# Performance work log

Measured on AMD Instinct MI355X. Metric: run time of the kernel, lower is better.

Reference implementation:

```python
import jax, jax.numpy as jnp
import numpy as np

B, T, H = 32, 4096, 1024

def setup_inputs() -> dict:
    key = jax.random.key(0)
    k1, k2 = jax.random.split(key)
    decoder_state = jax.random.normal(k1, (B, H), dtype=jnp.float32)
    encoder_hiddens = jax.random.normal(k2, (B, T, H), dtype=jnp.float32)
    return {"decoder_state": decoder_state, "encoder_hiddens": encoder_hiddens}

def reference(decoder_state, encoder_hiddens):
    # Faithful to the original: torch.sum(s_t * h_t) reduces over batch AND
    # hidden, so score[:, t] is one scalar broadcast to every batch row.
    # scores: [T]
    scores = jnp.einsum('bh,bth->t', decoder_state, encoder_hiddens)
    batch_size = encoder_hiddens.shape[0]
    attention_score = jnp.broadcast_to(scores[None, :], (batch_size, scores.shape[0]))
    attention_distribution = jax.nn.softmax(attention_score, axis=1)  # [B, T]
    # context_vector[b] = sum_t dist[b, t] * encoder_hiddens[b, t]
    context_vector = jnp.einsum('bt,bth->bh', attention_distribution, encoder_hiddens)
    return context_vector
```

## Files before the change

kernel.cpp:

```cpp
#include <hip/hip_runtime.h>
#include <math.h>

#define B_  32
#define T_  4096
#define H_  1024
#define H4_ 256
#define G_  256
#define TPG_ (T_ / G_)
#define BH4_ (B_ * H4_)

__global__ __launch_bounds__(1024) void flash_kernel(
    const float4* __restrict__ s4, const float4* __restrict__ eh4,
    float4* __restrict__ Og4, float* __restrict__ mg, float* __restrict__ lg)
{
    const int g    = blockIdx.x;
    const int tid  = threadIdx.x;
    const int lane = tid & 63;
    const int w    = tid >> 6;
    const int b    = tid >> 5;
    const int hb   = tid & 31;

    __shared__ float redw[16];
    __shared__ float sc_sh;

    float4 sreg[8];
#pragma unroll
    for (int j = 0; j < 8; ++j)
        sreg[j] = s4[b * H4_ + hb + 32 * j];

    const float4* ep = eh4 + ((size_t)b * T_ + (size_t)g * TPG_) * H4_ + hb;

    float4 acc[8];
#pragma unroll
    for (int j = 0; j < 8; ++j) acc[j] = make_float4(0.f, 0.f, 0.f, 0.f);
    float m = -INFINITY, l = 0.f;

    for (int i = 0; i < TPG_; ++i) {
        float4 e[8];
#pragma unroll
        for (int j = 0; j < 8; ++j) e[j] = ep[32 * j];
        ep += H4_;

        float p = 0.f;
#pragma unroll
        for (int j = 0; j < 8; ++j)
            p += e[j].x * sreg[j].x + e[j].y * sreg[j].y
               + e[j].z * sreg[j].z + e[j].w * sreg[j].w;

        for (int off = 32; off > 0; off >>= 1)
            p += __shfl_down(p, off, 64);
        if (lane == 0) redw[w] = p;
        __syncthreads();
        if (w == 0) {
            float q = (lane < 16) ? redw[lane] : 0.f;
            q += __shfl_down(q, 8, 64);
            q += __shfl_down(q, 4, 64);
            q += __shfl_down(q, 2, 64);
            q += __shfl_down(q, 1, 64);
            if (lane == 0) sc_sh = q;
        }
        __syncthreads();
        const float score = sc_sh;

        const float mn    = fmaxf(m, score);
        const float alpha = __expf(m - mn);
        const float wgt   = __expf(score - mn);
        l = l * alpha + wgt;
#pragma unroll
        for (int j = 0; j < 8; ++j) {
            acc[j].x = acc[j].x * alpha + wgt * e[j].x;
            acc[j].y = acc[j].y * alpha + wgt * e[j].y;
            acc[j].z = acc[j].z * alpha + wgt * e[j].z;
            acc[j].w = acc[j].w * alpha + wgt * e[j].w;
        }
        m = mn;
    }

    float4* op = Og4 + (size_t)g * BH4_ + b * H4_ + hb;
#pragma unroll
    for (int j = 0; j < 8; ++j) op[32 * j] = acc[j];
    if (tid == 0) { mg[g] = m; lg[g] = l; }
}

__global__ __launch_bounds__(64) void combine_kernel(
    const float4* __restrict__ Og4, const float* __restrict__ mg,
    const float* __restrict__ lg, float4* __restrict__ out4)
{
    const int tid = threadIdx.x;
    __shared__ float wsh[G_];

    float mv[4];
    float M = -INFINITY;
#pragma unroll
    for (int j = 0; j < 4; ++j) {
        mv[j] = mg[tid + 64 * j];
        M = fmaxf(M, mv[j]);
    }
    for (int off = 32; off > 0; off >>= 1)
        M = fmaxf(M, __shfl_down(M, off, 64));
    M = __shfl(M, 0, 64);

    float Ls = 0.f;
#pragma unroll
    for (int j = 0; j < 4; ++j)
        Ls += lg[tid + 64 * j] * __expf(mv[j] - M);
    for (int off = 32; off > 0; off >>= 1)
        Ls += __shfl_down(Ls, off, 64);
    Ls = __shfl(Ls, 0, 64);
    const float invL = 1.f / Ls;

#pragma unroll
    for (int j = 0; j < 4; ++j)
        wsh[tid + 64 * j] = __expf(mv[j] - M) * invL;
    __syncthreads();

    const int o4 = blockIdx.x * 64 + tid;
    float4 acc = make_float4(0.f, 0.f, 0.f, 0.f);
    for (int gg = 0; gg < G_; gg += 4) {
        float4 a0 = Og4[(size_t)(gg + 0) * BH4_ + o4];
        float4 a1 = Og4[(size_t)(gg + 1) * BH4_ + o4];
        float4 a2 = Og4[(size_t)(gg + 2) * BH4_ + o4];
        float4 a3 = Og4[(size_t)(gg + 3) * BH4_ + o4];
        float w0 = wsh[gg], w1 = wsh[gg + 1], w2 = wsh[gg + 2], w3 = wsh[gg + 3];
        acc.x += w0 * a0.x + w1 * a1.x + w2 * a2.x + w3 * a3.x;
        acc.y += w0 * a0.y + w1 * a1.y + w2 * a2.y + w3 * a3.y;
        acc.z += w0 * a0.z + w1 * a1.z + w2 * a2.z + w3 * a3.z;
        acc.w += w0 * a0.w + w1 * a1.w + w2 * a2.w + w3 * a3.w;
    }
    out4[o4] = acc;
}

extern "C" void kernel_launch(void* const* d_in, const int* in_sizes, int n_in,
                              void* d_out, int out_size, void* d_ws, size_t ws_size,
                              hipStream_t stream) {
    const float* s  = (const float*)d_in[0];
    const float* eh = (const float*)d_in[1];

    float4* Og4 = (float4*)d_ws;
    float*  mg  = (float*)(Og4 + (size_t)G_ * BH4_);
    float*  lg  = mg + G_;

    flash_kernel<<<G_, 1024, 0, stream>>>(
        (const float4*)s, (const float4*)eh, Og4, mg, lg);
    combine_kernel<<<BH4_ / 64, 64, 0, stream>>>(
        Og4, mg, lg, (float4*)d_out);
}
```

Before: 697.4 us.

## Pipeline score reduction with next-row prefetch, single barrier, and split combine

The flash kernel now makes each wavefront own two batch rows. It prefetches the next time step's encoder row into registers while the current row, staged in LDS, updates the accumulators. The two-barrier block reduction becomes one barrier over a double-buffered per-wave partial array that every thread reads and sums itself. The combine step is split into two kernels: one reduces chunks of partial outputs across many blocks, a second sums the chunks and normalises. This replaces the former 128-block combine that read all 256 partials serially. The changes add 128KB of LDS per block and an extra launch and workspace buffer.

```diff
diff --git a/kernel.cpp b/kernel.cpp
--- a/kernel.cpp
+++ b/kernel.cpp
@@ -1,13 +1,15 @@
 #include <hip/hip_runtime.h>
 #include <math.h>
 
-#define B_  32
-#define T_  4096
-#define H_  1024
-#define H4_ 256
-#define G_  256
+#define B_   32
+#define T_   4096
+#define H_   1024
+#define H4_  256
+#define G_   256
 #define TPG_ (T_ / G_)
 #define BH4_ (B_ * H4_)
+#define NCHUNK_ 8
+#define GPC_ (G_ / NCHUNK_)
 
 __global__ __launch_bounds__(1024) void flash_kernel(
     const float4* __restrict__ s4, const float4* __restrict__ eh4,
@@ -17,117 +19,185 @@
     const int tid  = threadIdx.x;
     const int lane = tid & 63;
     const int w    = tid >> 6;
-    const int b    = tid >> 5;
-    const int hb   = tid & 31;
-
-    __shared__ float redw[16];
-    __shared__ float sc_sh;
-
-    float4 sreg[8];
-#pragma unroll
-    for (int j = 0; j < 8; ++j)
-        sreg[j] = s4[b * H4_ + hb + 32 * j];
-
-    const float4* ep = eh4 + ((size_t)b * T_ + (size_t)g * TPG_) * H4_ + hb;
-
-    float4 acc[8];
-#pragma unroll
-    for (int j = 0; j < 8; ++j) acc[j] = make_float4(0.f, 0.f, 0.f, 0.f);
+    const int b0   = w * 2;
+    const int b1   = b0 + 1;
+
+    __shared__ float4 elds[B_ * H4_];
+    __shared__ __align__(16) float redw[2][16];
+
+    float4 sA[4], sB[4];
+#pragma unroll
+    for (int j = 0; j < 4; ++j) {
+        sA[j] = s4[b0 * H4_ + lane + 64 * j];
+        sB[j] = s4[b1 * H4_ + lane + 64 * j];
+    }
+
+    const float4* epA = eh4 + ((size_t)b0 * T_ + (size_t)g * TPG_) * H4_ + lane;
+    const float4* epB = eh4 + ((size_t)b1 * T_ + (size_t)g * TPG_) * H4_ + lane;
+    float4* slotA = &elds[b0 * H4_ + lane];
+    float4* slotB = &elds[b1 * H4_ + lane];
+
+    float pdot;
+    {
+        float4 eA[4], eB[4];
+#pragma unroll
+        for (int j = 0; j < 4; ++j) { eA[j] = epA[64 * j]; eB[j] = epB[64 * j]; }
+        epA += H4_; epB += H4_;
+        float p = 0.f;
+#pragma unroll
+        for (int j = 0; j < 4; ++j) {
+            p += eA[j].x * sA[j].x + eA[j].y * sA[j].y
+               + eA[j].z * sA[j].z + eA[j].w * sA[j].w;
+            p += eB[j].x * sB[j].x + eB[j].y * sB[j].y
+               + eB[j].z * sB[j].z + eB[j].w * sB[j].w;
+        }
+        pdot = p;
+#pragma unroll
+        for (int j = 0; j < 4; ++j) { slotA[64 * j] = eA[j]; slotB[64 * j] = eB[j]; }
+    }
+
+    float4 accA[4], accB[4];
+#pragma unroll
+    for (int j = 0; j < 4; ++j) {
+        accA[j] = make_float4(0.f, 0.f, 0.f, 0.f);
+        accB[j] = make_float4(0.f, 0.f, 0.f, 0.f);
+    }
     float m = -INFINITY, l = 0.f;
 
-    for (int i = 0; i < TPG_; ++i) {
-        float4 e[8];
-#pragma unroll
-        for (int j = 0; j < 8; ++j) e[j] = ep[32 * j];
-        ep += H4_;
-
-        float p = 0.f;
-#pragma unroll
-        for (int j = 0; j < 8; ++j)
-            p += e[j].x * sreg[j].x + e[j].y * sreg[j].y
-               + e[j].z * sreg[j].z + e[j].w * sreg[j].w;
-
+    for (int t = 0; t < TPG_; ++t) {
+        float4 eA[4], eB[4];
+        if (t < TPG_ - 1) {
+#pragma unroll
+            for (int j = 0; j < 4; ++j) { eA[j] = epA[64 * j]; eB[j] = epB[64 * j]; }
+            epA += H4_; epB += H4_;
+        }
+
+        float q = pdot;
         for (int off = 32; off > 0; off >>= 1)
-            p += __shfl_down(p, off, 64);
-        if (lane == 0) redw[w] = p;
-        __syncthreads();
-        if (w == 0) {
-            float q = (lane < 16) ? redw[lane] : 0.f;
-            q += __shfl_down(q, 8, 64);
-            q += __shfl_down(q, 4, 64);
-            q += __shfl_down(q, 2, 64);
-            q += __shfl_down(q, 1, 64);
-            if (lane == 0) sc_sh = q;
-        }
-        __syncthreads();
-        const float score = sc_sh;
+            q += __shfl_down(q, off, 64);
+        if (lane == 0) redw[t & 1][w] = q;
+        asm volatile("s_waitcnt lgkmcnt(0)" ::: "memory");
+        __builtin_amdgcn_sched_barrier(0);
+        __builtin_amdgcn_s_barrier();
+        __builtin_amdgcn_sched_barrier(0);
+        asm volatile("" ::: "memory");
+
+        const float4* rp = (const float4*)&redw[t & 1][0];
+        float4 r0 = rp[0], r1 = rp[1], r2 = rp[2], r3 = rp[3];
+        const float score = ((r0.x + r0.y) + (r0.z + r0.w))
+                          + ((r1.x + r1.y) + (r1.z + r1.w))
+                          + ((r2.x + r2.y) + (r2.z + r2.w))
+                          + ((r3.x + r3.y) + (r3.z + r3.w));
 
         const float mn    = fmaxf(m, score);
         const float alpha = __expf(m - mn);
         const float wgt   = __expf(score - mn);
         l = l * alpha + wgt;
-#pragma unroll
-        for (int j = 0; j < 8; ++j) {
-            acc[j].x = acc[j].x * alpha + wgt * e[j].x;
-            acc[j].y = acc[j].y * alpha + wgt * e[j].y;
-            acc[j].z = acc[j].z * alpha + wgt * e[j].z;
-            acc[j].w = acc[j].w * alpha + wgt * e[j].w;
-        }
         m = mn;
-    }
-
-    float4* op = Og4 + (size_t)g * BH4_ + b * H4_ + hb;
-#pragma unroll
-    for (int j = 0; j < 8; ++j) op[32 * j] = acc[j];
+
+#pragma unroll
+        for (int j = 0; j < 4; ++j) {
+            float4 vA = slotA[64 * j];
+            accA[j].x = accA[j].x * alpha + wgt * vA.x;
+            accA[j].y = accA[j].y * alpha + wgt * vA.y;
+            accA[j].z = accA[j].z * alpha + wgt * vA.z;
+            accA[j].w = accA[j].w * alpha + wgt * vA.w;
+            float4 vB = slotB[64 * j];
+            accB[j].x = accB[j].x * alpha + wgt * vB.x;
+            accB[j].y = accB[j].y * alpha + wgt * vB.y;
+            accB[j].z = accB[j].z * alpha + wgt * vB.z;
+            accB[j].w = accB[j].w * alpha + wgt * vB.w;
+        }
+
+        if (t < TPG_ - 1) {
+            float p1 = 0.f;
+#pragma unroll
+            for (int j = 0; j < 4; ++j) {
+                p1 += eA[j].x * sA[j].x + eA[j].y * sA[j].y
+                    + eA[j].z * sA[j].z + eA[j].w * sA[j].w;
+                p1 += eB[j].x * sB[j].x + eB[j].y * sB[j].y
+                    + eB[j].z * sB[j].z + eB[j].w * sB[j].w;
+            }
+            pdot = p1;
+#pragma unroll
+            for (int j = 0; j < 4; ++j) { slotA[64 * j] = eA[j]; slotB[64 * j] = eB[j]; }
+        }
+    }
+
+    float4* opA = Og4 + (size_t)g * BH4_ + b0 * H4_ + lane;
+    float4* opB = Og4 + (size_t)g * BH4_ + b1 * H4_ + lane;
+#pragma unroll
+    for (int j = 0; j < 4; ++j) { opA[64 * j] = accA[j]; opB[64 * j] = accB[j]; }
     if (tid == 0) { mg[g] = m; lg[g] = l; }
 }
 
-__global__ __launch_bounds__(64) void combine_kernel(
+__global__ __launch_bounds__(256) void combine_a(
     const float4* __restrict__ Og4, const float* __restrict__ mg,
+    float4* __restrict__ p2)
+{
+    const int tid = threadIdx.x;
+    const int oc  = blockIdx.x & 31;
+    const int gc  = blockIdx.x >> 5;
+    __shared__ float wsh[GPC_];
+    __shared__ float red[4];
+
+    float mv = mg[tid];
+    float M = mv;
+    for (int off = 32; off > 0; off >>= 1)
+        M = fmaxf(M, __shfl_down(M, off, 64));
+    if ((tid & 63) == 0) red[tid >> 6] = M;
+    __syncthreads();
+    M = fmaxf(fmaxf(red[0], red[1]), fmaxf(red[2], red[3]));
+    __syncthreads();
+
+    if (tid < GPC_) wsh[tid] = __expf(mg[gc * GPC_ + tid] - M);
+    __syncthreads();
+
+    const int o4 = oc * 256 + tid;
+    const float4* src = Og4 + (size_t)(gc * GPC_) * BH4_ + o4;
+    float4 acc = make_float4(0.f, 0.f, 0.f, 0.f);
+#pragma unroll 8
+    for (int gg = 0; gg < GPC_; ++gg) {
+        float4 a = src[(size_t)gg * BH4_];
+        float wv = wsh[gg];
+        acc.x += wv * a.x; acc.y += wv * a.y;
+        acc.z += wv * a.z; acc.w += wv * a.w;
+    }
+    p2[(size_t)gc * BH4_ + o4] = acc;
+}
+
+__global__ __launch_bounds__(256) void combine_b(
+    const float4* __restrict__ p2, const float* __restrict__ mg,
     const float* __restrict__ lg, float4* __restrict__ out4)
 {
     const int tid = threadIdx.x;
-    __shared__ float wsh[G_];
-
-    float mv[4];
-    float M = -INFINITY;
-#pragma unroll
-    for (int j = 0; j < 4; ++j) {
-        mv[j] = mg[tid + 64 * j];
-        M = fmaxf(M, mv[j]);
-    }
+    __shared__ float red[4];
+
+    float mv = mg[tid];
+    float M = mv;
     for (int off = 32; off > 0; off >>= 1)
         M = fmaxf(M, __shfl_down(M, off, 64));
-    M = __shfl(M, 0, 64);
-
-    float Ls = 0.f;
-#pragma unroll
-    for (int j = 0; j < 4; ++j)
-        Ls += lg[tid + 64 * j] * __expf(mv[j] - M);
+    if ((tid & 63) == 0) red[tid >> 6] = M;
+    __syncthreads();
+    M = fmaxf(fmaxf(red[0], red[1]), fmaxf(red[2], red[3]));
+    __syncthreads();
+
+    float Ls = lg[tid] * __expf(mv - M);
     for (int off = 32; off > 0; off >>= 1)
         Ls += __shfl_down(Ls, off, 64);
-    Ls = __shfl(Ls, 0, 64);
-    const float invL = 1.f / Ls;
-
-#pragma unroll
-    for (int j = 0; j < 4; ++j)
-        wsh[tid + 64 * j] = __expf(mv[j] - M) * invL;
-    __syncthreads();
-
-    const int o4 = blockIdx.x * 64 + tid;
+    if ((tid & 63) == 0) red[tid >> 6] = Ls;
+    __syncthreads();
+    const float invL = 1.f / ((red[0] + red[1]) + (red[2] + red[3]));
+
+    const int o4 = blockIdx.x * 256 + tid;
     float4 acc = make_float4(0.f, 0.f, 0.f, 0.f);
-    for (int gg = 0; gg < G_; gg += 4) {
-        float4 a0 = Og4[(size_t)(gg + 0) * BH4_ + o4];
-        float4 a1 = Og4[(size_t)(gg + 1) * BH4_ + o4];
-        float4 a2 = Og4[(size_t)(gg + 2) * BH4_ + o4];
-        float4 a3 = Og4[(size_t)(gg + 3) * BH4_ + o4];
-        float w0 = wsh[gg], w1 = wsh[gg + 1], w2 = wsh[gg + 2], w3 = wsh[gg + 3];
-        acc.x += w0 * a0.x + w1 * a1.x + w2 * a2.x + w3 * a3.x;
-        acc.y += w0 * a0.y + w1 * a1.y + w2 * a2.y + w3 * a3.y;
-        acc.z += w0 * a0.z + w1 * a1.z + w2 * a2.z + w3 * a3.z;
-        acc.w += w0 * a0.w + w1 * a1.w + w2 * a2.w + w3 * a3.w;
-    }
-    out4[o4] = acc;
+#pragma unroll
+    for (int gc = 0; gc < NCHUNK_; ++gc) {
+        float4 a = p2[(size_t)gc * BH4_ + o4];
+        acc.x += a.x; acc.y += a.y; acc.z += a.z; acc.w += a.w;
+    }
+    out4[o4] = make_float4(acc.x * invL, acc.y * invL,
+                           acc.z * invL, acc.w * invL);
 }
 
 extern "C" void kernel_launch(void* const* d_in, const int* in_sizes, int n_in,
@@ -137,11 +207,12 @@
     const float* eh = (const float*)d_in[1];
 
     float4* Og4 = (float4*)d_ws;
-    float*  mg  = (float*)(Og4 + (size_t)G_ * BH4_);
+    float*  mg  = (float*)((char*)d_ws + (size_t)G_ * BH4_ * 16);
     float*  lg  = mg + G_;
+    float4* p2  = (float4*)((char*)d_ws + (size_t)G_ * BH4_ * 16 + 4096);
 
     flash_kernel<<<G_, 1024, 0, stream>>>(
         (const float4*)s, (const float4*)eh, Og4, mg, lg);
-    combine_kernel<<<BH4_ / 64, 64, 0, stream>>>(
-        Og4, mg, lg, (float4*)d_out);
-}
+    combine_a<<<G_, 256, 0, stream>>>(Og4, mg, p2);
+    combine_b<<<BH4_ / 256, 256, 0, stream>>>(p2, mg, lg, (float4*)d_out);
+}
```

Result: no change. 702.0 us (+0.7%).

## Split flash attention into score, softmax, and context passes with more parallel blocks

Applied to the files above, without the earlier changes.

Replaces the single-pass online-softmax kernel with four kernels: per-batch partial scores, a single-block global softmax, a chunked weighted sum over encoder hiddens, and a chunk-combine. It removes the two per-row block barriers and the large partial-output combine, and exposes more independent blocks to stream memory. In exchange, the encoder hiddens tensor is read twice and there are extra launches, including a serial single-block softmax.

```diff
diff --git a/kernel.cpp b/kernel.cpp
--- a/kernel.cpp
+++ b/kernel.cpp
@@ -1,131 +1,144 @@
 #include <hip/hip_runtime.h>
 #include <math.h>
 
-#define B_  32
-#define T_  4096
-#define H_  1024
-#define H4_ 256
-#define G_  256
-#define TPG_ (T_ / G_)
-#define BH4_ (B_ * H4_)
+#define B_    32
+#define T_    4096
+#define H_    1024
+#define H4_   256
+#define NC_   32
+#define CH_   (T_ / NC_)
+#define WPT_  (CH_ / 4)
 
-__global__ __launch_bounds__(1024) void flash_kernel(
+
+__global__ __launch_bounds__(256) void score_kernel(
     const float4* __restrict__ s4, const float4* __restrict__ eh4,
-    float4* __restrict__ Og4, float* __restrict__ mg, float* __restrict__ lg)
+    float* __restrict__ psc)
 {
-    const int g    = blockIdx.x;
+    const int blk  = blockIdx.x;
+    const int b    = blk >> 5;
+    const int c    = blk & 31;
     const int tid  = threadIdx.x;
     const int lane = tid & 63;
     const int w    = tid >> 6;
-    const int b    = tid >> 5;
-    const int hb   = tid & 31;
 
-    __shared__ float redw[16];
-    __shared__ float sc_sh;
+    float4 sreg[4];
+#pragma unroll
+    for (int j = 0; j < 4; ++j)
+        sreg[j] = s4[b * H4_ + lane + 64 * j];
 
-    float4 sreg[8];
-#pragma unroll
-    for (int j = 0; j < 8; ++j)
-        sreg[j] = s4[b * H4_ + hb + 32 * j];
+    const int tbase = c * CH_ + w * WPT_;
+    const float4* rowp = eh4 + ((size_t)b * T_ + tbase) * H4_ + lane;
 
-    const float4* ep = eh4 + ((size_t)b * T_ + (size_t)g * TPG_) * H4_ + hb;
+    float4 c0 = rowp[0], c1 = rowp[64], c2 = rowp[128], c3 = rowp[192];
 
-    float4 acc[8];
-#pragma unroll
-    for (int j = 0; j < 8; ++j) acc[j] = make_float4(0.f, 0.f, 0.f, 0.f);
-    float m = -INFINITY, l = 0.f;
+    for (int i = 0; i < WPT_; ++i) {
+        float4 n0, n1, n2, n3;
+        if (i < WPT_ - 1) {
+            rowp += H4_;
+            n0 = rowp[0]; n1 = rowp[64]; n2 = rowp[128]; n3 = rowp[192];
+        }
 
-    for (int i = 0; i < TPG_; ++i) {
-        float4 e[8];
-#pragma unroll
-        for (int j = 0; j < 8; ++j) e[j] = ep[32 * j];
-        ep += H4_;
-
-        float p = 0.f;
-#pragma unroll
-        for (int j = 0; j < 8; ++j)
-            p += e[j].x * sreg[j].x + e[j].y * sreg[j].y
-               + e[j].z * sreg[j].z + e[j].w * sreg[j].w;
-
+        float p = c0.x * sreg[0].x + c0.y * sreg[0].y
+                + c0.z * sreg[0].z + c0.w * sreg[0].w
+                + c1.x * sreg[1].x + c1.y * sreg[1].y
+                + c1.z * sreg[1].z + c1.w * sreg[1].w
+                + c2.x * sreg[2].x + c2.y * sreg[2].y
+                + c2.z * sreg[2].z + c2.w * sreg[2].w
+                + c3.x * sreg[3].x + c3.y * sreg[3].y
+                + c3.z * sreg[3].z + c3.w * sreg[3].w;
         for (int off = 32; off > 0; off >>= 1)
             p += __shfl_down(p, off, 64);
-        if (lane == 0) redw[w] = p;
-        __syncthreads();
-        if (w == 0) {
-            float q = (lane < 16) ? redw[lane] : 0.f;
-            q += __shfl_down(q, 8, 64);
-            q += __shfl_down(q, 4, 64);
-            q += __shfl_down(q, 2, 64);
-            q += __shfl_down(q, 1, 64);
-            if (lane == 0) sc_sh = q;
-        }
-        __syncthreads();
-        const float score = sc_sh;
+        if (lane == 0) psc[(size_t)(tbase + i) * B_ + b] = p;
 
-        const float mn    = fmaxf(m, score);
-        const float alpha = __expf(m - mn);
-        const float wgt   = __expf(score - mn);
-        l = l * alpha + wgt;
+        if (i < WPT_ - 1) { c0 = n0; c1 = n1; c2 = n2; c3 = n3; }
+    }
+}
+
+__global__ __launch_bounds__(1024) void softmax_kernel(
+    const float* __restrict__ psc, float* __restrict__ wout)
+{
+    const int tid  = threadIdx.x;
+    const int lane = tid & 63;
+    const int w    = tid >> 6;
+    __shared__ float red[16];
+
+    float s[4];
+#pragma unroll
+    for (int k = 0; k < 4; ++k) {
+        const float4* pp = (const float4*)psc + (size_t)(tid + 1024 * k) * 8;
+        float acc = 0.f;
 #pragma unroll
         for (int j = 0; j < 8; ++j) {
-            acc[j].x = acc[j].x * alpha + wgt * e[j].x;
-            acc[j].y = acc[j].y * alpha + wgt * e[j].y;
-            acc[j].z = acc[j].z * alpha + wgt * e[j].z;
-            acc[j].w = acc[j].w * alpha + wgt * e[j].w;
+            float4 a = pp[j];
+            acc += (a.x + a.y) + (a.z + a.w);
         }
-        m = mn;
+        s[k] = acc;
     }
 
-    float4* op = Og4 + (size_t)g * BH4_ + b * H4_ + hb;
+    float M = fmaxf(fmaxf(s[0], s[1]), fmaxf(s[2], s[3]));
+    for (int off = 32; off > 0; off >>= 1)
+        M = fmaxf(M, __shfl_down(M, off, 64));
+    if (lane == 0) red[w] = M;
+    __syncthreads();
+    float Mg = -INFINITY;
 #pragma unroll
-    for (int j = 0; j < 8; ++j) op[32 * j] = acc[j];
-    if (tid == 0) { mg[g] = m; lg[g] = l; }
+    for (int j = 0; j < 16; ++j) Mg = fmaxf(Mg, red[j]);
+    __syncthreads();
+
+    float e[4];
+    float ls = 0.f;
+#pragma unroll
+    for (int k = 0; k < 4; ++k) { e[k] = __expf(s[k] - Mg); ls += e[k]; }
+    for (int off = 32; off > 0; off >>= 1)
+        ls += __shfl_down(ls, off, 64);
+    if (lane == 0) red[w] = ls;
+    __syncthreads();
+    float Lg = 0.f;
+#pragma unroll
+    for (int j = 0; j < 16; ++j) Lg += red[j];
+    const float inv = 1.f / Lg;
+
+#pragma unroll
+    for (int k = 0; k < 4; ++k) wout[tid + 1024 * k] = e[k] * inv;
 }
 
-__global__ __launch_bounds__(64) void combine_kernel(
-    const float4* __restrict__ Og4, const float* __restrict__ mg,
-    const float* __restrict__ lg, float4* __restrict__ out4)
+__global__ __launch_bounds__(256) void ctx_kernel(
+    const float4* __restrict__ eh4, const float* __restrict__ wv,
+    float4* __restrict__ op4)
 {
+    const int blk = blockIdx.x;
+    const int b   = blk >> 5;
+    const int c   = blk & 31;
     const int tid = threadIdx.x;
-    __shared__ float wsh[G_];
 
-    float mv[4];
-    float M = -INFINITY;
-#pragma unroll
-    for (int j = 0; j < 4; ++j) {
-        mv[j] = mg[tid + 64 * j];
-        M = fmaxf(M, mv[j]);
-    }
-    for (int off = 32; off > 0; off >>= 1)
-        M = fmaxf(M, __shfl_down(M, off, 64));
-    M = __shfl(M, 0, 64);
-
-    float Ls = 0.f;
-#pragma unroll
-    for (int j = 0; j < 4; ++j)
-        Ls += lg[tid + 64 * j] * __expf(mv[j] - M);
-    for (int off = 32; off > 0; off >>= 1)
-        Ls += __shfl_down(Ls, off, 64);
-    Ls = __shfl(Ls, 0, 64);
-    const float invL = 1.f / Ls;
-
-#pragma unroll
-    for (int j = 0; j < 4; ++j)
-        wsh[tid + 64 * j] = __expf(mv[j] - M) * invL;
+    __shared__ float wl[CH_];
+    if (tid < CH_) wl[tid] = wv[c * CH_ + tid];
     __syncthreads();
 
-    const int o4 = blockIdx.x * 64 + tid;
+    const float4* p = eh4 + ((size_t)b * T_ + c * CH_) * H4_ + tid;
     float4 acc = make_float4(0.f, 0.f, 0.f, 0.f);
-    for (int gg = 0; gg < G_; gg += 4) {
-        float4 a0 = Og4[(size_t)(gg + 0) * BH4_ + o4];
-        float4 a1 = Og4[(size_t)(gg + 1) * BH4_ + o4];
-        float4 a2 = Og4[(size_t)(gg + 2) * BH4_ + o4];
-        float4 a3 = Og4[(size_t)(gg + 3) * BH4_ + o4];
-        float w0 = wsh[gg], w1 = wsh[gg + 1], w2 = wsh[gg + 2], w3 = wsh[gg + 3];
-        acc.x += w0 * a0.x + w1 * a1.x + w2 * a2.x + w3 * a3.x;
-        acc.y += w0 * a0.y + w1 * a1.y + w2 * a2.y + w3 * a3.y;
-        acc.z += w0 * a0.z + w1 * a1.z + w2 * a2.z + w3 * a3.z;
-        acc.w += w0 * a0.w + w1 * a1.w + w2 * a2.w + w3 * a3.w;
+#pragma unroll 8
+    for (int t = 0; t < CH_; ++t) {
+        float4 a = p[(size_t)t * H4_];
+        const float ww = wl[t];
+        acc.x += ww * a.x; acc.y += ww * a.y;
+        acc.z += ww * a.z; acc.w += ww * a.w;
+    }
+    op4[((size_t)b * NC_ + c) * H4_ + tid] = acc;
+}
+
+__global__ __launch_bounds__(256) void comb_kernel(
+    const float4* __restrict__ op4, float4* __restrict__ out4)
+{
+    const int o4 = blockIdx.x * 256 + threadIdx.x;
+    const int b  = o4 >> 8;
+    const int h4 = o4 & 255;
+    const float4* p = op4 + (size_t)b * NC_ * H4_ + h4;
+    float4 acc = make_float4(0.f, 0.f, 0.f, 0.f);
+#pragma unroll 8
+    for (int c = 0; c < NC_; ++c) {
+        float4 a = p[(size_t)c * H4_];
+        acc.x += a.x; acc.y += a.y; acc.z += a.z; acc.w += a.w;
     }
     out4[o4] = acc;
 }
@@ -136,12 +149,13 @@
     const float* s  = (const float*)d_in[0];
     const float* eh = (const float*)d_in[1];
 
-    float4* Og4 = (float4*)d_ws;
-    float*  mg  = (float*)(Og4 + (size_t)G_ * BH4_);
-    float*  lg  = mg + G_;
+    float* psc = (float*)d_ws;
+    float* wv  = psc + (size_t)T_ * B_;
+    float4* op = (float4*)((char*)d_ws + (1 << 20));
 
-    flash_kernel<<<G_, 1024, 0, stream>>>(
-        (const float4*)s, (const float4*)eh, Og4, mg, lg);
-    combine_kernel<<<BH4_ / 64, 64, 0, stream>>>(
-        Og4, mg, lg, (float4*)d_out);
+    score_kernel<<<B_ * NC_, 256, 0, stream>>>(
+        (const float4*)s, (const float4*)eh, psc);
+    softmax_kernel<<<1, 1024, 0, stream>>>(psc, wv);
+    ctx_kernel<<<B_ * NC_, 256, 0, stream>>>((const float4*)eh, wv, op);
+    comb_kernel<<<(B_ * H4_) / 256, 256, 0, stream>>>(op, (float4*)d_out);
 }
```

Result: slower. 790.2 us (+13.3%).
